# Kernel tuning notes

Hardware: AMD Instinct MI355X
Metric: run time of the kernel (lower is better)

The kernel has to match this reference:

```python
import jax, jax.numpy as jnp
import numpy as np

B, N, K, H = 8192, 512, 8, 1024  # batch, size_half, n_segments, hidden width


def setup_inputs() -> dict:
    key = jax.random.key(0)
    ks = jax.random.split(key, 8)
    out_dim = N * (2 * K + 1)  # 8704
    v_in = jax.random.uniform(ks[0], (B, 2 * N), jnp.float32)  # in [0,1]
    log_density = jax.random.uniform(ks[1], (B, 1), jnp.float32)
    W1 = jax.random.normal(ks[2], (N, H), jnp.float32) / np.float32(np.sqrt(N))
    b1 = jnp.zeros((H,), jnp.float32)
    W2 = jax.random.normal(ks[3], (H, H), jnp.float32) / np.float32(np.sqrt(H))
    b2 = jnp.zeros((H,), jnp.float32)
    W3 = jax.random.normal(ks[4], (H, out_dim), jnp.float32) / np.float32(np.sqrt(H))
    b3 = jnp.zeros((out_dim,), jnp.float32)
    return {"v_in": v_in, "log_density": log_density,
            "W1": W1, "b1": b1, "W2": W2, "b2": b2, "W3": W3, "b3": b3}


def reference(v_in, log_density, W1, b1, W2, b2, W3, b3):
    v_passive = v_in[:, :N]   # even_sites=True -> passive first
    v_active = v_in[:, N:]
    # fully connected net, tanh on every layer (no_final_activation=False)
    x = jnp.tanh((v_passive - 0.5) @ W1 + b1)
    x = jnp.tanh(x @ W2 + b2)
    x = jnp.tanh(x @ W3 + b3)
    net = x.reshape(B, N, 2 * K + 1)
    h_net, w_net = net[..., : K + 1], net[..., K + 1 :]
    w_norm = jax.nn.softmax(w_net, axis=2)                          # (B,N,K)
    eh = jnp.exp(h_net)                                             # (B,N,K+1)
    denom = (0.5 * w_norm * (eh[..., :-1] + eh[..., 1:])).sum(axis=2, keepdims=True)
    h_norm = eh / denom                                             # (B,N,K+1)
    zeros = jnp.zeros((B, N, 1), v_in.dtype)
    knots_x = jnp.concatenate([zeros, jnp.cumsum(w_norm, axis=2)], axis=2)  # (B,N,K+1)
    knots_y = jnp.concatenate(
        [zeros, jnp.cumsum(0.5 * w_norm * (h_norm[..., :-1] + h_norm[..., 1:]), axis=2)],
        axis=2)                                                     # (B,N,K+1)
    # left-searchsorted(knots_x, v_active) == count of knots strictly below v
    k = jnp.clip(jnp.sum(knots_x < v_active[..., None], axis=2) - 1, 0, K - 1)  # (B,N)
    idx = k[..., None]
    w_seg = jnp.take_along_axis(w_norm, idx, axis=2)[..., 0]
    h_lo = jnp.take_along_axis(h_norm, idx, axis=2)[..., 0]
    h_hi = jnp.take_along_axis(h_norm, idx + 1, axis=2)[..., 0]
    x_lo = jnp.take_along_axis(knots_x, idx, axis=2)[..., 0]
    y_lo = jnp.take_along_axis(knots_y, idx, axis=2)[..., 0]
    alpha = (v_active - x_lo) / w_seg
    v_active_out = y_lo + alpha * h_lo * w_seg + 0.5 * alpha ** 2 * (h_hi - h_lo) * w_seg
    v_out = jnp.concatenate([v_passive, v_active_out], axis=1)      # (B,2N)
    log_density_out = log_density - jnp.log(h_lo + alpha * (h_hi - h_lo)).sum(axis=1, keepdims=True)
    return v_out, log_density_out
```

## Files before the change

### kernel.cpp

```cpp
#include <hip/hip_runtime.h>
#include <math.h>

#define BB    8192
#define NN    512
#define KKN   8
#define HH    1024
#define OUTD  (NN * (2 * KKN + 1))

typedef unsigned short ushort_t;
typedef __bf16 bf16x8 __attribute__((ext_vector_type(8)));
typedef float  f32x16 __attribute__((ext_vector_type(16)));
typedef float  f32x4  __attribute__((ext_vector_type(4)));
typedef int    i32x4  __attribute__((ext_vector_type(4)));
typedef float  f32x2v __attribute__((ext_vector_type(2)));

__device__ inline ushort_t f2bf(float f) {
    unsigned int u = __float_as_uint(f);
    unsigned int r = (u + 0x7fffu + ((u >> 16) & 1u)) >> 16;
    return (ushort_t)r;
}
__device__ inline float bf2f(ushort_t u) {
    return __uint_as_float(((unsigned int)u) << 16);
}

__device__ inline float fast_tanh(float x) {
    float t = __expf(x + x);
    return fmaf(-2.f, __builtin_amdgcn_rcpf(t + 1.f), 1.f);
}

__global__ __launch_bounds__(256) void conv_v(
    const float* __restrict__ v_in, ushort_t* __restrict__ a0b)
{
    int t = blockIdx.x * 256 + threadIdx.x;
    int e0 = t * 2;
    int b = e0 >> 9;
    int n = e0 & 511;
    const float2 v = *(const float2*)(v_in + (size_t)b * (2 * NN) + n);
    ushort_t* o = a0b + (size_t)b * NN + n;
    o[0] = f2bf(v.x - 0.5f);
    o[1] = f2bf(v.y - 0.5f);
}

template <bool PERM>
__global__ __launch_bounds__(256) void transpose_cvt(
    const float* __restrict__ W, ushort_t* __restrict__ WT, int Kd, int Nd)
{
    __shared__ float tile[32][33];
    const int bx = blockIdx.x * 32;
    const int by = blockIdx.y * 32;
    const int tx = threadIdx.x;
    const int ty = threadIdx.y;
#pragma unroll
    for (int i = 0; i < 32; i += 8)
        tile[ty + i][tx] = W[(size_t)(by + ty + i) * Nd + bx + tx];
    __syncthreads();
#pragma unroll
    for (int i = 0; i < 32; i += 8) {
        int r = bx + ty + i;
        if (PERM) r = (r % 17) * 512 + (r / 17);
        WT[(size_t)r * Kd + by + tx] = f2bf(tile[tx][ty + i]);
    }
}

template <bool PERM_BIAS>
__global__ __launch_bounds__(256) void gemm_bt_tanh(
    const ushort_t* __restrict__ A,
    const ushort_t* __restrict__ BT,
    const float* __restrict__ bias,
    ushort_t* __restrict__ C,
    int N_, int K)
{
    __shared__ __align__(16) ushort_t sA[128 * 32];
    __shared__ __align__(16) ushort_t sB[128 * 32];

    const int t    = threadIdx.x;
    const int lane = t & 63;
    const int w    = t >> 6;
    const int wy   = w >> 1;
    const int wx   = w & 1;
    const int l31  = lane & 31;
    const int h    = lane >> 5;

    const int brow = blockIdx.y * 128;
    const int bcol = blockIdx.x * 128;

    f32x16 acc[2][2] = {};

    const int cwb = (t & ~63);

    int rS[2], gS[2];
#pragma unroll
    for (int p = 0; p < 2; ++p) {
        const int c = p * 256 + t;
        rS[p] = c >> 2;
        gS[p] = ((c & 3) - (rS[p] >> 1)) & 3;
    }

    int offA[2][2], offB[2][2];
#pragma unroll
    for (int ks = 0; ks < 2; ++ks)
#pragma unroll
        for (int ti = 0; ti < 2; ++ti) {
            const int rA = wy * 64 + ti * 32 + l31;
            offA[ks][ti] = rA * 32 + ((2 * ks + h + (rA >> 1)) & 3) * 8;
            const int rB = wx * 64 + ti * 32 + l31;
            offB[ks][ti] = rB * 32 + ((2 * ks + h + (rB >> 1)) & 3) * 8;
        }

    for (int k0 = 0; k0 < K; k0 += 32) {
        __syncthreads();
#pragma unroll
        for (int p = 0; p < 2; ++p) {
            const int cb = p * 256 + cwb;
            const ushort_t* ga = A  + (size_t)(brow + rS[p]) * K + k0 + gS[p] * 8;
            const ushort_t* gb = BT + (size_t)(bcol + rS[p]) * K + k0 + gS[p] * 8;
            __builtin_amdgcn_global_load_lds(
                (const __attribute__((address_space(1))) void*)ga,
                (__attribute__((address_space(3))) void*)(sA + (size_t)cb * 8), 16, 0, 0);
            __builtin_amdgcn_global_load_lds(
                (const __attribute__((address_space(1))) void*)gb,
                (__attribute__((address_space(3))) void*)(sB + (size_t)cb * 8), 16, 0, 0);
        }
        __syncthreads();

#pragma unroll
        for (int ks = 0; ks < 2; ++ks) {
            const bf16x8 a0 = *(const bf16x8*)(sA + offA[ks][0]);
            const bf16x8 a1 = *(const bf16x8*)(sA + offA[ks][1]);
            const bf16x8 b0 = *(const bf16x8*)(sB + offB[ks][0]);
            const bf16x8 b1 = *(const bf16x8*)(sB + offB[ks][1]);
            acc[0][0] = __builtin_amdgcn_mfma_f32_32x32x16_bf16(a0, b0, acc[0][0], 0, 0, 0);
            acc[0][1] = __builtin_amdgcn_mfma_f32_32x32x16_bf16(a0, b1, acc[0][1], 0, 0, 0);
            acc[1][0] = __builtin_amdgcn_mfma_f32_32x32x16_bf16(a1, b0, acc[1][0], 0, 0, 0);
            acc[1][1] = __builtin_amdgcn_mfma_f32_32x32x16_bf16(a1, b1, acc[1][1], 0, 0, 0);
        }
    }

#pragma unroll
    for (int tj = 0; tj < 2; ++tj) {
        const int col = bcol + wx * 64 + tj * 32 + l31;
        const int bidx = PERM_BIAS ? ((col & 511) * 17 + (col >> 9)) : col;
        const float bv = bias[bidx];
#pragma unroll
        for (int ti = 0; ti < 2; ++ti) {
            const int rb = brow + wy * 64 + ti * 32 + 4 * h;
#pragma unroll
            for (int reg = 0; reg < 16; ++reg) {
                const int row = rb + (reg & 3) + 8 * (reg >> 2);
                C[(size_t)row * N_ + col] = f2bf(fast_tanh(acc[ti][tj][reg] + bv));
            }
        }
    }
}

#define SLOT_U (256 * 32)

__device__ __forceinline__ void stage16(
    const ushort_t* __restrict__ gsrc, ushort_t* lds_dst)
{
    __builtin_amdgcn_global_load_lds(
        (const __attribute__((address_space(1))) void*)gsrc,
        (__attribute__((address_space(3))) void*)lds_dst, 16, 0, 0);
}

template <bool PERM_BIAS>
__global__ __launch_bounds__(512, 2) void gemm3_bt_tanh_256(
    const ushort_t* __restrict__ A,
    const ushort_t* __restrict__ BT,
    const float* __restrict__ bias,
    ushort_t* __restrict__ C,
    int N_, int K)
{
    __shared__ __align__(16) ushort_t smem[8 * SLOT_U];
    ushort_t* sA = smem;
    ushort_t* sB = smem + 4 * SLOT_U;

    const int t    = threadIdx.x;
    const int lane = t & 63;
    const int w    = t >> 6;
    const int wy   = w >> 2;
    const int wx   = w & 3;
    const int l15  = lane & 15;
    const int kg   = lane >> 4;

    const int gx = gridDim.x, gy = gridDim.y;
    int br, bc;
    {
        const int o = blockIdx.y * gx + blockIdx.x;
        if ((gy & 7) == 0) {
            const int rpx = gy >> 3;
            const int xcd = o & 7;
            const int seq = o >> 3;
            const int bpg = rpx << 3;
            const int g   = seq / bpg;
            const int rem = seq % bpg;
            const int gcw = gx - g * 8;
            const int gw  = gcw < 8 ? gcw : 8;
            bc = g * 8 + rem % gw;
            br = xcd * rpx + rem / gw;
        } else {
            const int nwg = gx * gy;
            const int id = (o & 7) * (nwg >> 3) + (o >> 3);
            br = id / gx; bc = id % gx;
        }
    }
    const int brow = br * 256;
    const int bcol = bc * 256;

    f32x4 acc[8][4] = {};

    const int rL  = t >> 2;
    const int g8  = (((t & 3) ^ ((t >> 3) & 3)) << 3);
    const int wbU = (t & ~63) * 8;
    const size_t rowA0 = (size_t)(brow + rL) * K;
    const size_t rowA1 = (size_t)(brow + 128 + rL) * K;
    const size_t rowB0 = (size_t)(bcol + rL) * K;
    const size_t rowB1 = (size_t)(bcol + 128 + rL) * K;

    int offA[8], offB[4];
#pragma unroll
    for (int m = 0; m < 8; ++m) {
        const int r = wy * 128 + m * 16 + l15;
        offA[m] = r * 32 + (((kg ^ (r >> 1)) & 3) << 3);
    }
#pragma unroll
    for (int n = 0; n < 4; ++n) {
        const int r = wx * 64 + n * 16 + l15;
        offB[n] = r * 32 + (((kg ^ (r >> 1)) & 3) << 3);
    }

    const int NT = K >> 5;

#pragma unroll
    for (int sp = 0; sp < 3; ++sp) {
        const int kk = sp << 5;
        ushort_t* dA = sA + sp * SLOT_U + wbU;
        ushort_t* dB = sB + sp * SLOT_U + wbU;
        stage16(A  + rowA0 + kk + g8, dA);
        stage16(BT + rowB0 + kk + g8, dB);
        stage16(A  + rowA1 + kk + g8, dA + 4096);
        stage16(BT + rowB1 + kk + g8, dB + 4096);
    }
    asm volatile("s_waitcnt vmcnt(8)" ::: "memory");
    __builtin_amdgcn_s_barrier();

    for (int s = 0; s < NT; ++s) {
        const ushort_t* sAs = sA + (s & 3) * SLOT_U;
        const ushort_t* sBs = sB + (s & 3) * SLOT_U;
        const int sp = s + 3;
        const int kk = sp << 5;
        ushort_t* dA = sA + (sp & 3) * SLOT_U + wbU;
        ushort_t* dB = sB + (sp & 3) * SLOT_U + wbU;

        bf16x8 bR[4], aR[8];
#pragma unroll
        for (int n = 0; n < 4; ++n) bR[n] = *(const bf16x8*)(sBs + offB[n]);
#pragma unroll
        for (int m = 0; m < 8; ++m) aR[m] = *(const bf16x8*)(sAs + offA[m]);

        if (sp < NT) {
            stage16(A  + rowA0 + kk + g8, dA);
            stage16(BT + rowB0 + kk + g8, dB);
            stage16(A  + rowA1 + kk + g8, dA + 4096);
            stage16(BT + rowB1 + kk + g8, dB + 4096);
        }

#pragma unroll
        for (int m = 0; m < 8; ++m)
#pragma unroll
            for (int n = 0; n < 4; ++n)
                acc[m][n] = __builtin_amdgcn_mfma_f32_16x16x32_bf16(
                    aR[m], bR[n], acc[m][n], 0, 0, 0);

        if (s < NT - 3)       asm volatile("s_waitcnt vmcnt(8)" ::: "memory");
        else if (s == NT - 3) asm volatile("s_waitcnt vmcnt(4)" ::: "memory");
        else if (s == NT - 2) asm volatile("s_waitcnt vmcnt(0)" ::: "memory");
        __builtin_amdgcn_s_barrier();
    }

    ushort_t* sC = smem;
#pragma unroll
    for (int n = 0; n < 4; ++n) {
        const int cg  = wx * 64 + n * 16 + l15;
        const int col = bcol + cg;
        const int bidx = PERM_BIAS ? ((col & 511) * 17 + (col >> 9)) : col;
        const float bv = bias[bidx];
#pragma unroll
        for (int m = 0; m < 8; ++m) {
            const int rg0 = wy * 128 + m * 16 + kg * 4;
            const int cgs = cg ^ (((rg0 >> 2) & 3) << 4);
#pragma unroll
            for (int reg = 0; reg < 4; ++reg)
                sC[(rg0 + reg) * 256 + cgs] =
                    f2bf(fast_tanh(acc[m][n][reg] + bv));
        }
    }
    __syncthreads();

#pragma unroll
    for (int i = 0; i < 16; ++i) {
        const int slot = i * 512 + t;
        const int r  = slot >> 5;
        const int j  = slot & 31;
        const int js = j ^ (((r >> 2) & 3) << 1);
        const i32x4 v = *(const i32x4*)(sC + r * 256 + js * 8);
        __builtin_nontemporal_store(
            v, (i32x4*)(C + (size_t)(brow + r) * N_ + bcol + j * 8));
    }
}

__global__ __launch_bounds__(256) void spline_post(
    const ushort_t* __restrict__ net,
    const float* __restrict__ v_in,
    const float* __restrict__ ld_in,
    float* __restrict__ v_out,
    float* __restrict__ ld_out)
{
    const int b = blockIdx.x;
    const int t = threadIdx.x;

    unsigned int pl[17];
    const ushort_t* base = net + (size_t)b * OUTD + 2 * t;
#pragma unroll
    for (int p = 0; p < 17; ++p)
        pl[p] = __builtin_nontemporal_load((const unsigned int*)(base + p * 512));

    {
        const f32x2v vp = __builtin_nontemporal_load(
            (const f32x2v*)(v_in + (size_t)b * (2 * NN) + 2 * t));
        __builtin_nontemporal_store(
            vp, (f32x2v*)(v_out + (size_t)b * (2 * NN) + 2 * t));
    }
    const f32x2v va2 = __builtin_nontemporal_load(
        (const f32x2v*)(v_in + (size_t)b * (2 * NN) + NN + 2 * t));

    float vact[2];
    float lt_sum = 0.f;
#pragma unroll 1
    for (int u = 0; u < 2; ++u) {
        const int sh = u * 16;
        float t17[17];
#pragma unroll
        for (int p = 0; p < 17; ++p)
            t17[p] = bf2f((ushort_t)(pl[p] >> sh));

        float m = t17[9];
#pragma unroll
        for (int i = 10; i < 17; i++) m = fmaxf(m, t17[i]);
        float wn[8], wsum = 0.f;
#pragma unroll
        for (int i = 0; i < 8; i++) { wn[i] = __expf(t17[9 + i] - m); wsum += wn[i]; }
        const float winv = 1.f / wsum;
#pragma unroll
        for (int i = 0; i < 8; i++) wn[i] *= winv;

        float eh[9];
#pragma unroll
        for (int i = 0; i < 9; i++) eh[i] = __expf(t17[i]);
        float denom = 0.f;
#pragma unroll
        for (int k = 0; k < 8; k++) denom += 0.5f * wn[k] * (eh[k] + eh[k + 1]);
        const float dinv = 1.f / denom;
        float hn[9];
#pragma unroll
        for (int i = 0; i < 9; i++) hn[i] = eh[i] * dinv;

        float kx[9], ky[9];
        kx[0] = 0.f; ky[0] = 0.f;
#pragma unroll
        for (int k = 0; k < 8; k++) {
            kx[k + 1] = kx[k] + wn[k];
            ky[k + 1] = ky[k] + 0.5f * wn[k] * (hn[k] + hn[k + 1]);
        }

        const float va = (u == 0) ? va2.x : va2.y;
        int cnt = 0;
#pragma unroll
        for (int j = 0; j < 9; j++) cnt += (kx[j] < va) ? 1 : 0;
        int k = cnt - 1;
        k = k < 0 ? 0 : (k > KKN - 1 ? KKN - 1 : k);

        const float wseg = wn[k];
        const float hlo = hn[k], hhi = hn[k + 1];
        const float xlo = kx[k], ylo = ky[k];
        const float alpha = (va - xlo) / wseg;
        vact[u] = ylo + alpha * hlo * wseg + 0.5f * alpha * alpha * (hhi - hlo) * wseg;
        lt_sum += __logf(hlo + alpha * (hhi - hlo));
    }

    {
        f32x2v vo; vo.x = vact[0]; vo.y = vact[1];
        __builtin_nontemporal_store(
            vo, (f32x2v*)(v_out + (size_t)b * (2 * NN) + NN + 2 * t));
    }

    __shared__ float wred[4];
#pragma unroll
    for (int o = 32; o > 0; o >>= 1) lt_sum += __shfl_down(lt_sum, o, 64);
    if ((t & 63) == 0) wred[t >> 6] = lt_sum;
    __syncthreads();
    if (t == 0)
        ld_out[b] = ld_in[b] - (wred[0] + wred[1] + wred[2] + wred[3]);
}

extern "C" void kernel_launch(void* const* d_in, const int* in_sizes, int n_in,
                              void* d_out, int out_size, void* d_ws, size_t ws_size,
                              hipStream_t stream)
{
    const float* v_in = (const float*)d_in[0];
    const float* ld   = (const float*)d_in[1];
    const float* W1   = (const float*)d_in[2];
    const float* b1   = (const float*)d_in[3];
    const float* W2   = (const float*)d_in[4];
    const float* b2   = (const float*)d_in[5];
    const float* W3   = (const float*)d_in[6];
    const float* b3   = (const float*)d_in[7];

    float* out    = (float*)d_out;
    float* v_out  = out;
    float* ld_out = out + (size_t)BB * (2 * NN);

    const size_t Mi = 1048576;
    int    chunk;
    size_t region;
    if      (ws_size >= 172 * Mi) { chunk = 8192; region = 136 * Mi; }
    else if (ws_size >= 104 * Mi) { chunk = 4096; region =  68 * Mi; }
    else if (ws_size >=  70 * Mi) { chunk = 2048; region =  34 * Mi; }
    else                          { chunk = 1024; region =  24 * Mi; }

    char* ws = (char*)d_ws;
    ushort_t* a0b = (ushort_t*)(ws);
    ushort_t* x1b = (ushort_t*)(ws + 8 * Mi);
    ushort_t* netc = (ushort_t*)(ws);
    ushort_t* x2b = (ushort_t*)(ws + region);
    ushort_t* W1T = (ushort_t*)(ws + region + 16 * Mi);
    ushort_t* W2T = (ushort_t*)(ws + region + 17 * Mi);
    ushort_t* W3T = (ushort_t*)(ws + region + 19 * Mi);

    conv_v<<<dim3(BB * NN / 2 / 256), dim3(256), 0, stream>>>(v_in, a0b);
    transpose_cvt<false><<<dim3(HH / 32, NN / 32),   dim3(32, 8), 0, stream>>>(W1, W1T, NN, HH);
    transpose_cvt<false><<<dim3(HH / 32, HH / 32),   dim3(32, 8), 0, stream>>>(W2, W2T, HH, HH);
    transpose_cvt<true ><<<dim3(OUTD / 32, HH / 32), dim3(32, 8), 0, stream>>>(W3, W3T, HH, OUTD);

    gemm_bt_tanh<false><<<dim3(HH / 128, BB / 128), dim3(256), 0, stream>>>(
        a0b, W1T, b1, x1b, HH, NN);
    gemm_bt_tanh<false><<<dim3(HH / 128, BB / 128), dim3(256), 0, stream>>>(
        x1b, W2T, b2, x2b, HH, HH);

    for (int c = 0; c < BB / chunk; ++c) {
        const ushort_t* xa = x2b + (size_t)c * chunk * HH;
        gemm3_bt_tanh_256<true><<<dim3(OUTD / 256, chunk / 256), dim3(512), 0, stream>>>(
            xa, W3T, b3, netc, OUTD, HH);
        spline_post<<<dim3(chunk), dim3(256), 0, stream>>>(
            netc,
            v_in   + (size_t)c * chunk * (2 * NN),
            ld     + (size_t)c * chunk,
            v_out  + (size_t)c * chunk * (2 * NN),
            ld_out + (size_t)c * chunk);
    }
}
```

Baseline: 383.9 us.

## Double-buffer LDS-to-register fragments to overlap ds_reads with MFMA in GEMM loop

The GEMM main loop is unrolled by two and uses two register fragment sets (aF/bF and aG/bG). The next k-step's fragments are read from LDS while the current step's MFMAs run. The global-to-LDS prefetch schedule and the vmcnt waits are retuned to match the new ordering. This trades higher VGPR pressure for hiding LDS read latency behind matrix instructions. The loop also assumes NT is even, and the barrier and wait placement gets more delicate.

```diff
diff --git a/kernel.cpp b/kernel.cpp
--- a/kernel.cpp
+++ b/kernel.cpp
@@ -241,40 +241,72 @@
         stage16(A  + rowA1 + kk + g8, dA + 4096);
         stage16(BT + rowB1 + kk + g8, dB + 4096);
     }
-    asm volatile("s_waitcnt vmcnt(8)" ::: "memory");
+    asm volatile("s_waitcnt vmcnt(4)" ::: "memory");
     __builtin_amdgcn_s_barrier();
 
-    for (int s = 0; s < NT; ++s) {
-        const ushort_t* sAs = sA + (s & 3) * SLOT_U;
-        const ushort_t* sBs = sB + (s & 3) * SLOT_U;
-        const int sp = s + 3;
-        const int kk = sp << 5;
-        ushort_t* dA = sA + (sp & 3) * SLOT_U + wbU;
-        ushort_t* dB = sB + (sp & 3) * SLOT_U + wbU;
-
-        bf16x8 bR[4], aR[8];
-#pragma unroll
-        for (int n = 0; n < 4; ++n) bR[n] = *(const bf16x8*)(sBs + offB[n]);
-#pragma unroll
-        for (int m = 0; m < 8; ++m) aR[m] = *(const bf16x8*)(sAs + offA[m]);
-
-        if (sp < NT) {
+    bf16x8 aF[8], bF[4];
+    bf16x8 aG[8], bG[4];
+#pragma unroll
+    for (int n = 0; n < 4; ++n) bF[n] = *(const bf16x8*)(sB + offB[n]);
+#pragma unroll
+    for (int m = 0; m < 8; ++m) aF[m] = *(const bf16x8*)(sA + offA[m]);
+
+    for (int s = 0; s < NT; s += 2) {
+        {
+            const ushort_t* nA = sA + ((s + 1) & 3) * SLOT_U;
+            const ushort_t* nB = sB + ((s + 1) & 3) * SLOT_U;
+#pragma unroll
+            for (int n = 0; n < 4; ++n) bG[n] = *(const bf16x8*)(nB + offB[n]);
+#pragma unroll
+            for (int m = 0; m < 8; ++m) aG[m] = *(const bf16x8*)(nA + offA[m]);
+        }
+        if (s + 3 < NT) {
+            const int kk = (s + 3) << 5;
+            ushort_t* dA = sA + ((s + 3) & 3) * SLOT_U + wbU;
+            ushort_t* dB = sB + ((s + 3) & 3) * SLOT_U + wbU;
             stage16(A  + rowA0 + kk + g8, dA);
             stage16(BT + rowB0 + kk + g8, dB);
             stage16(A  + rowA1 + kk + g8, dA + 4096);
             stage16(BT + rowB1 + kk + g8, dB + 4096);
         }
-
 #pragma unroll
         for (int m = 0; m < 8; ++m)
 #pragma unroll
             for (int n = 0; n < 4; ++n)
                 acc[m][n] = __builtin_amdgcn_mfma_f32_16x16x32_bf16(
-                    aR[m], bR[n], acc[m][n], 0, 0, 0);
-
-        if (s < NT - 3)       asm volatile("s_waitcnt vmcnt(8)" ::: "memory");
-        else if (s == NT - 3) asm volatile("s_waitcnt vmcnt(4)" ::: "memory");
-        else if (s == NT - 2) asm volatile("s_waitcnt vmcnt(0)" ::: "memory");
+                    aF[m], bF[n], acc[m][n], 0, 0, 0);
+        if (s < NT - 3)       asm volatile("s_waitcnt vmcnt(4)" ::: "memory");
+        else if (s == NT - 3) asm volatile("s_waitcnt vmcnt(0)" ::: "memory");
+        __builtin_amdgcn_s_barrier();
+
+        if (s + 2 < NT) {
+            const ushort_t* nA = sA + ((s + 2) & 3) * SLOT_U;
+            const ushort_t* nB = sB + ((s + 2) & 3) * SLOT_U;
+#pragma unroll
+            for (int n = 0; n < 4; ++n) bF[n] = *(const bf16x8*)(nB + offB[n]);
+#pragma unroll
+            for (int m = 0; m < 8; ++m) aF[m] = *(const bf16x8*)(nA + offA[m]);
+        }
+        if (s + 4 < NT) {
+            const int kk = (s + 4) << 5;
+            ushort_t* dA = sA + ((s + 4) & 3) * SLOT_U + wbU;
+            ushort_t* dB = sB + ((s + 4) & 3) * SLOT_U + wbU;
+            stage16(A  + rowA0 + kk + g8, dA);
+            stage16(BT + rowB0 + kk + g8, dB);
+            stage16(A  + rowA1 + kk + g8, dA + 4096);
+            stage16(BT + rowB1 + kk + g8, dB + 4096);
+        }
+#pragma unroll
+        for (int m = 0; m < 8; ++m)
+#pragma unroll
+            for (int n = 0; n < 4; ++n)
+                acc[m][n] = __builtin_amdgcn_mfma_f32_16x16x32_bf16(
+                    aG[m], bG[n], acc[m][n], 0, 0, 0);
+        {
+            const int s1 = s + 1;
+            if (s1 < NT - 3)       asm volatile("s_waitcnt vmcnt(4)" ::: "memory");
+            else if (s1 == NT - 3) asm volatile("s_waitcnt vmcnt(0)" ::: "memory");
+        }
         __builtin_amdgcn_s_barrier();
     }
 
```

New measurement: 385.0 us. About the same (+0.3%).

## Shrink layer-3 GEMM tile to 128x256 and drop multi-stage LDS pipeline

Applied to the files above, without the earlier changes.

The third-layer GEMM now uses a 128x256 output tile instead of 256x256, with fewer accumulators per wave and launch bounds asking for 4 blocks per CU. The 4-slot asynchronous LDS prefetch pipeline is replaced by single-buffer staging with two barriers per K step. Epilogue stores to the output switch from nontemporal to plain stores. The intent is higher occupancy to hide latency, at the cost of less data reuse per tile, no load/compute overlap inside a block, and more barriers.

```diff
diff --git a/kernel.cpp b/kernel.cpp
--- a/kernel.cpp
+++ b/kernel.cpp
@@ -153,8 +153,6 @@
     }
 }
 
-#define SLOT_U (256 * 32)
-
 __device__ __forceinline__ void stage16(
     const ushort_t* __restrict__ gsrc, ushort_t* lds_dst)
 {
@@ -164,16 +162,16 @@
 }
 
 template <bool PERM_BIAS>
-__global__ __launch_bounds__(512, 2) void gemm3_bt_tanh_256(
+__global__ __launch_bounds__(512, 4) void gemm3_bt_tanh_128x256(
     const ushort_t* __restrict__ A,
     const ushort_t* __restrict__ BT,
     const float* __restrict__ bias,
     ushort_t* __restrict__ C,
     int N_, int K)
 {
-    __shared__ __align__(16) ushort_t smem[8 * SLOT_U];
+    __shared__ __align__(16) ushort_t smem[128 * 256];
     ushort_t* sA = smem;
-    ushort_t* sB = smem + 4 * SLOT_U;
+    ushort_t* sB = smem + 4096;
 
     const int t    = threadIdx.x;
     const int lane = t & 63;
@@ -204,23 +202,22 @@
             br = id / gx; bc = id % gx;
         }
     }
-    const int brow = br * 256;
+    const int brow = br * 128;
     const int bcol = bc * 256;
 
-    f32x4 acc[8][4] = {};
-
-    const int rL  = t >> 2;
+    f32x4 acc[4][4] = {};
+
+    const int rT  = t >> 2;
     const int g8  = (((t & 3) ^ ((t >> 3) & 3)) << 3);
     const int wbU = (t & ~63) * 8;
-    const size_t rowA0 = (size_t)(brow + rL) * K;
-    const size_t rowA1 = (size_t)(brow + 128 + rL) * K;
-    const size_t rowB0 = (size_t)(bcol + rL) * K;
-    const size_t rowB1 = (size_t)(bcol + 128 + rL) * K;
-
-    int offA[8], offB[4];
-#pragma unroll
-    for (int m = 0; m < 8; ++m) {
-        const int r = wy * 128 + m * 16 + l15;
+    const size_t rowA  = (size_t)(brow + rT) * K;
+    const size_t rowB0 = (size_t)(bcol + rT) * K;
+    const size_t rowB1 = (size_t)(bcol + 128 + rT) * K;
+
+    int offA[4], offB[4];
+#pragma unroll
+    for (int m = 0; m < 4; ++m) {
+        const int r = wy * 64 + m * 16 + l15;
         offA[m] = r * 32 + (((kg ^ (r >> 1)) & 3) << 3);
     }
 #pragma unroll
@@ -229,54 +226,26 @@
         offB[n] = r * 32 + (((kg ^ (r >> 1)) & 3) << 3);
     }
 
-    const int NT = K >> 5;
-
-#pragma unroll
-    for (int sp = 0; sp < 3; ++sp) {
-        const int kk = sp << 5;
-        ushort_t* dA = sA + sp * SLOT_U + wbU;
-        ushort_t* dB = sB + sp * SLOT_U + wbU;
-        stage16(A  + rowA0 + kk + g8, dA);
-        stage16(BT + rowB0 + kk + g8, dB);
-        stage16(A  + rowA1 + kk + g8, dA + 4096);
-        stage16(BT + rowB1 + kk + g8, dB + 4096);
-    }
-    asm volatile("s_waitcnt vmcnt(8)" ::: "memory");
-    __builtin_amdgcn_s_barrier();
-
-    for (int s = 0; s < NT; ++s) {
-        const ushort_t* sAs = sA + (s & 3) * SLOT_U;
-        const ushort_t* sBs = sB + (s & 3) * SLOT_U;
-        const int sp = s + 3;
-        const int kk = sp << 5;
-        ushort_t* dA = sA + (sp & 3) * SLOT_U + wbU;
-        ushort_t* dB = sB + (sp & 3) * SLOT_U + wbU;
-
-        bf16x8 bR[4], aR[8];
-#pragma unroll
-        for (int n = 0; n < 4; ++n) bR[n] = *(const bf16x8*)(sBs + offB[n]);
-#pragma unroll
-        for (int m = 0; m < 8; ++m) aR[m] = *(const bf16x8*)(sAs + offA[m]);
-
-        if (sp < NT) {
-            stage16(A  + rowA0 + kk + g8, dA);
-            stage16(BT + rowB0 + kk + g8, dB);
-            stage16(A  + rowA1 + kk + g8, dA + 4096);
-            stage16(BT + rowB1 + kk + g8, dB + 4096);
-        }
-
-#pragma unroll
-        for (int m = 0; m < 8; ++m)
+    for (int k0 = 0; k0 < K; k0 += 32) {
+        __syncthreads();
+        stage16(A  + rowA  + k0 + g8, sA + wbU);
+        stage16(BT + rowB0 + k0 + g8, sB + wbU);
+        stage16(BT + rowB1 + k0 + g8, sB + 4096 + wbU);
+        __syncthreads();
+
+        bf16x8 aR[4], bR[4];
+#pragma unroll
+        for (int n = 0; n < 4; ++n) bR[n] = *(const bf16x8*)(sB + offB[n]);
+#pragma unroll
+        for (int m = 0; m < 4; ++m) aR[m] = *(const bf16x8*)(sA + offA[m]);
+#pragma unroll
+        for (int m = 0; m < 4; ++m)
 #pragma unroll
             for (int n = 0; n < 4; ++n)
                 acc[m][n] = __builtin_amdgcn_mfma_f32_16x16x32_bf16(
                     aR[m], bR[n], acc[m][n], 0, 0, 0);
-
-        if (s < NT - 3)       asm volatile("s_waitcnt vmcnt(8)" ::: "memory");
-        else if (s == NT - 3) asm volatile("s_waitcnt vmcnt(4)" ::: "memory");
-        else if (s == NT - 2) asm volatile("s_waitcnt vmcnt(0)" ::: "memory");
-        __builtin_amdgcn_s_barrier();
-    }
+    }
+    __syncthreads();
 
     ushort_t* sC = smem;
 #pragma unroll
@@ -286,8 +255,8 @@
         const int bidx = PERM_BIAS ? ((col & 511) * 17 + (col >> 9)) : col;
         const float bv = bias[bidx];
 #pragma unroll
-        for (int m = 0; m < 8; ++m) {
-            const int rg0 = wy * 128 + m * 16 + kg * 4;
+        for (int m = 0; m < 4; ++m) {
+            const int rg0 = wy * 64 + m * 16 + kg * 4;
             const int cgs = cg ^ (((rg0 >> 2) & 3) << 4);
 #pragma unroll
             for (int reg = 0; reg < 4; ++reg)
@@ -298,14 +267,13 @@
     __syncthreads();
 
 #pragma unroll
-    for (int i = 0; i < 16; ++i) {
+    for (int i = 0; i < 8; ++i) {
         const int slot = i * 512 + t;
         const int r  = slot >> 5;
         const int j  = slot & 31;
         const int js = j ^ (((r >> 2) & 3) << 1);
-        const i32x4 v = *(const i32x4*)(sC + r * 256 + js * 8);
-        __builtin_nontemporal_store(
-            v, (i32x4*)(C + (size_t)(brow + r) * N_ + bcol + j * 8));
+        *(i32x4*)(C + (size_t)(brow + r) * N_ + bcol + j * 8) =
+            *(const i32x4*)(sC + r * 256 + js * 8);
     }
 }
 
@@ -449,7 +417,7 @@
 
     for (int c = 0; c < BB / chunk; ++c) {
         const ushort_t* xa = x2b + (size_t)c * chunk * HH;
-        gemm3_bt_tanh_256<true><<<dim3(OUTD / 256, chunk / 256), dim3(512), 0, stream>>>(
+        gemm3_bt_tanh_128x256<true><<<dim3(OUTD / 256, chunk / 128), dim3(512), 0, stream>>>(
             xa, W3T, b3, netc, OUTD, HH);
         spline_post<<<dim3(chunk), dim3(256), 0, stream>>>(
             netc,
```

Result: slower. 395.3 us (+3.0%).
